# Optimization experiments

Hardware: AMD Instinct MI355X
Metric: run time of the kernel (lower is better)

The kernel has to match this reference:

```python
import jax, jax.numpy as jnp
import numpy as np

K_NEIGHBORS = 5
WEIGHT = 0.5
EPS = 1e-12


def _l2_normalize(x):
    return x / jnp.maximum(jnp.linalg.norm(x, axis=1, keepdims=True), EPS)


def setup_inputs() -> dict:
    key = jax.random.key(0)
    k1, k2, k3, k4 = jax.random.split(key, 4)
    return {
        "hidden_current": jax.random.normal(k1, (4096, 768), dtype=jnp.float32),
        "hidden_previous": jax.random.normal(k2, (8192, 768), dtype=jnp.float32),
        "labels_current": jax.random.randint(k3, (4096,), 0, 100, dtype=jnp.int64),
        "labels_previous": jax.random.randint(k4, (8192,), 0, 100, dtype=jnp.int64),
    }


def reference(hidden_current, hidden_previous, labels_current, labels_previous):
    B_curr = hidden_current.shape[0]
    B_prev = hidden_previous.shape[0]

    # --- affinity from previous representations (no_grad in original) ---
    hp = _l2_normalize(jax.lax.stop_gradient(hidden_previous))
    dist_prev = 1.0 - hp @ hp.T                      # [B_prev, B_prev] cosine distance
    # smallest k+1 distances == largest k+1 of negated distances
    _, nbr = jax.lax.top_k(-dist_prev, K_NEIGHBORS + 1)
    nbr = nbr[:, 1:]                                 # drop self, [B_prev, K]
    same = labels_previous[:, None] == labels_previous[nbr]   # [B_prev, K]
    e = jnp.where(same, 1.0, -1.0).astype(jnp.float32)        # w - b
    rows = jnp.arange(B_prev)[:, None]
    affinity = jnp.zeros((B_prev, B_prev), dtype=jnp.float32).at[rows, nbr].set(e)

    # --- squared pairwise distances of normalized current representations ---
    hc = _l2_normalize(hidden_current)
    sq = jnp.sum(hc * hc, axis=1)
    d2 = jnp.maximum(sq[:, None] + sq[None, :] - 2.0 * (hc @ hc.T), 0.0)  # [B_curr, B_curr]

    loss = jnp.sum(affinity[:B_curr, :B_curr] * d2) / (B_curr * B_curr)
    return WEIGHT * loss
```

## Files before the change

kernel.cpp:

```cpp
#include <hip/hip_runtime.h>

#define BC 4096
#define BP 8192
#define D  768
#define KNB 5
#define TOPK 6
#define NT (BP / 128)

typedef __bf16 bf16x8 __attribute__((ext_vector_type(8)));
typedef float  f32x4  __attribute__((ext_vector_type(4)));

__device__ __forceinline__ unsigned short f2bf(float f) {
    unsigned int u = __float_as_uint(f);
    u += 0x7fffu + ((u >> 16) & 1u);
    return (unsigned short)(u >> 16);
}

__device__ __forceinline__ void gload16(const void* g, void* l) {
    __builtin_amdgcn_global_load_lds(
        (const __attribute__((address_space(1))) unsigned int*)g,
        (__attribute__((address_space(3))) unsigned int*)l, 16, 0, 0);
}

__device__ __forceinline__ void topk_insert(float v, int j, float* bv, int* bj) {
    #pragma unroll
    for (int q = TOPK - 1; q >= 1; q--) {
        bool up   = v > bv[q - 1];
        bool here = (v > bv[q]) && !up;
        bv[q] = up ? bv[q - 1] : (here ? v : bv[q]);
        bj[q] = up ? bj[q - 1] : (here ? j : bj[q]);
    }
    if (v > bv[0]) { bv[0] = v; bj[0] = j; }
}

__global__ __launch_bounds__(256) void k_norm(const float* __restrict__ hp,
                                              const float* __restrict__ hc,
                                              unsigned short* __restrict__ hpnb,
                                              float* __restrict__ hcn,
                                              float* __restrict__ sqout,
                                              float* __restrict__ out) {
    int b = blockIdx.x;
    int t = threadIdx.x;
    if (b == 0 && t == 0) out[0] = 0.0f;
    bool isP = (b < BP);
    int row = isP ? b : (b - BP);
    const float* xr = (isP ? hp : hc) + (size_t)row * D;
    float v0 = xr[t], v1 = xr[t + 256], v2 = xr[t + 512];
    float s = v0 * v0 + v1 * v1 + v2 * v2;
    #pragma unroll
    for (int off = 32; off; off >>= 1) s += __shfl_xor(s, off, 64);
    __shared__ float wsum[4];
    if ((t & 63) == 0) wsum[t >> 6] = s;
    __syncthreads();
    float tot = wsum[0] + wsum[1] + wsum[2] + wsum[3];
    float rinv = 1.0f / fmaxf(sqrtf(tot), 1e-12f);
    if (isP) {
        unsigned short* yr = hpnb + (size_t)row * D;
        int rx = (row & 7) << 3;
        yr[t ^ rx]         = f2bf(v0 * rinv);
        yr[(t + 256) ^ rx] = f2bf(v1 * rinv);
        yr[(t + 512) ^ rx] = f2bf(v2 * rinv);
    } else {
        float* yr = hcn + (size_t)row * D;
        yr[t] = v0 * rinv; yr[t + 256] = v1 * rinv; yr[t + 512] = v2 * rinv;
        if (t == 0) sqout[row] = tot * rinv * rinv;
    }
}

__global__ __launch_bounds__(256, 3) void k_simtop(const unsigned short* __restrict__ hp,
                                                   float* __restrict__ candv,
                                                   int* __restrict__ candi) {
    __shared__ char smem[39424];
    unsigned short* sA = (unsigned short*)smem;
    unsigned short* sB = sA + 128 * 64;
    float* sS = (float*)smem;
    float* mv = (float*)(smem + 33280);
    int*   mj = (int*)(smem + 33280 + 3072);

    const int t = threadIdx.x;
    const int l = t & 63;
    const int w = t >> 6;
    const int l15 = l & 15, quad = l >> 4;
    const int wr = w >> 1, wc = w & 1;

    int ri, ci;
    {
        int b = blockIdx.x;
        int super_id = (((b >> 9) & 3) << 3) | (b & 7);
        int within = (b >> 3) & 63;
        ri = (super_id >> 3) * 8 + (within >> 3);
        ci = (super_id & 7) * 8 + (within & 7);
    }

    const int srow = l >> 3, sch = l & 7;
    const unsigned short* Ag = hp + (size_t)(ri * 128 + w * 32 + srow) * D + sch * 8;
    const unsigned short* Bg = hp + (size_t)(ci * 128 + w * 32 + srow) * D + sch * 8;
    unsigned short* la = sA + (w * 32) * 64;
    unsigned short* lb = sB + (w * 32) * 64;

    f32x4 acc[4][4];
    #pragma unroll
    for (int i = 0; i < 4; i++)
        #pragma unroll
        for (int j = 0; j < 4; j++) acc[i][j] = (f32x4){0.f, 0.f, 0.f, 0.f};

    const int x7  = l15 & 7;
    const int ch0 = (quad ^ x7) * 16;
    const int ch1 = ((quad + 4) ^ x7) * 16;

    for (int kk = 0; kk < D; kk += 64) {
        __syncthreads();
        #pragma unroll
        for (int p = 0; p < 4; p++) {
            gload16(Ag + (size_t)(p * 8) * D + kk, la + (p * 8) * 64);
            gload16(Bg + (size_t)(p * 8) * D + kk, lb + (p * 8) * 64);
        }
        __syncthreads();
        #pragma unroll
        for (int ks = 0; ks < 2; ks++) {
            const int ch = ks ? ch1 : ch0;
            bf16x8 af[4], bfr[4];
            #pragma unroll
            for (int mi = 0; mi < 4; mi++)
                af[mi] = *(const bf16x8*)((const char*)sA + (wr * 64 + mi * 16 + l15) * 128 + ch);
            #pragma unroll
            for (int ni = 0; ni < 4; ni++)
                bfr[ni] = *(const bf16x8*)((const char*)sB + (wc * 64 + ni * 16 + l15) * 128 + ch);
            #pragma unroll
            for (int mi = 0; mi < 4; mi++)
                #pragma unroll
                for (int ni = 0; ni < 4; ni++)
                    acc[mi][ni] = __builtin_amdgcn_mfma_f32_16x16x32_bf16(af[mi], bfr[ni], acc[mi][ni], 0, 0, 0);
        }
    }

    float bv[TOPK]; int bj[TOPK];
    #pragma unroll
    for (int s = 0; s < TOPK; s++) { bv[s] = -1e30f; bj[s] = 0x7fffffff; }

    const int erow = t & 127, scb = (t >> 7) * 32;
    #pragma unroll
    for (int h = 0; h < 2; h++) {
        __syncthreads();
        if (wc == h) {
            #pragma unroll
            for (int mi = 0; mi < 4; mi++)
                #pragma unroll
                for (int ni = 0; ni < 4; ni++) {
                    int colb = ni * 16 + l15;
                    int rowb = wr * 64 + mi * 16 + quad * 4;
                    f32x4 v = acc[mi][ni];
                    #pragma unroll
                    for (int r = 0; r < 4; r++) sS[(rowb + r) * 65 + colb] = v[r];
                }
        }
        __syncthreads();
        int jbase = ci * 128 + h * 64 + scb;
        for (int c = 0; c < 32; c++) {
            float v = sS[erow * 65 + scb + c];
            if (v > bv[TOPK - 1]) topk_insert(v, jbase + c, bv, bj);
        }
    }

    __syncthreads();
    if (t >= 128) {
        #pragma unroll
        for (int s = 0; s < TOPK; s++) { mv[(t - 128) * TOPK + s] = bv[s]; mj[(t - 128) * TOPK + s] = bj[s]; }
    }
    __syncthreads();
    if (t < 128) {
        #pragma unroll
        for (int s0 = 0; s0 < TOPK; s0++) {
            float v = mv[t * TOPK + s0];
            if (v > bv[TOPK - 1]) topk_insert(v, mj[t * TOPK + s0], bv, bj);
        }
        size_t o = ((size_t)(ri * 128 + t) * NT + ci) * TOPK;
        #pragma unroll
        for (int s = 0; s < TOPK; s++) { candv[o + s] = bv[s]; candi[o + s] = bj[s]; }
    }
}

__global__ __launch_bounds__(256) void k_mergeloss(const float* __restrict__ candv,
                                                   const int* __restrict__ candi,
                                                   const float* __restrict__ hcn,
                                                   const float* __restrict__ sq,
                                                   const int* __restrict__ labp,
                                                   float* __restrict__ out) {
    __shared__ float bsum[4];
    const int w = threadIdx.x >> 6, lane = threadIdx.x & 63;
    const int i = blockIdx.x * 4 + w;

    const float* cv = candv + ((size_t)i * NT + lane) * TOPK;
    const int*   cj = candi + ((size_t)i * NT + lane) * TOPK;
    float bv[TOPK]; int bj[TOPK];
    #pragma unroll
    for (int s = 0; s < TOPK; s++) { bv[s] = cv[s]; bj[s] = cj[s]; }

    #pragma unroll
    for (int off = 1; off < 64; off <<= 1) {
        float pv[TOPK]; int pj[TOPK];
        #pragma unroll
        for (int s = 0; s < TOPK; s++) {
            pv[s] = __shfl_xor(bv[s], off, 64);
            pj[s] = __shfl_xor(bj[s], off, 64);
        }
        bool ilow = (lane & off) == 0;
        float av[TOPK], iv[TOPK]; int aj[TOPK], ij[TOPK];
        #pragma unroll
        for (int s = 0; s < TOPK; s++) {
            av[s] = ilow ? bv[s] : pv[s];  aj[s] = ilow ? bj[s] : pj[s];
            iv[s] = ilow ? pv[s] : bv[s];  ij[s] = ilow ? pj[s] : bj[s];
        }
        #pragma unroll
        for (int s = 0; s < TOPK; s++)
            if (iv[s] > av[TOPK - 1]) topk_insert(iv[s], ij[s], av, aj);
        #pragma unroll
        for (int s = 0; s < TOPK; s++) { bv[s] = av[s]; bj[s] = aj[s]; }
    }

    const float* hi = hcn + (size_t)i * D;
    float4 h0 = *(const float4*)(hi + lane * 4);
    float4 h1 = *(const float4*)(hi + lane * 4 + 256);
    float4 h2 = *(const float4*)(hi + lane * 4 + 512);
    float sqi = sq[i];
    int li = labp[i];
    float part = 0.f;
    float base = 0.f;
    #pragma unroll
    for (int s = 1; s <= KNB; s++) {
        int j = bj[s];
        if (j >= BC) continue;
        const float* hj = hcn + (size_t)j * D;
        float4 g0 = *(const float4*)(hj + lane * 4);
        float4 g1 = *(const float4*)(hj + lane * 4 + 256);
        float4 g2 = *(const float4*)(hj + lane * 4 + 512);
        float d = h0.x * g0.x + h0.y * g0.y + h0.z * g0.z + h0.w * g0.w
                + h1.x * g1.x + h1.y * g1.y + h1.z * g1.z + h1.w * g1.w
                + h2.x * g2.x + h2.y * g2.y + h2.z * g2.z + h2.w * g2.w;
        float e = (li == labp[j]) ? 1.0f : -1.0f;
        part += e * (-2.0f) * d;
        if (lane == 0) base += e * (sqi + sq[j]);
    }
    part += base;
    #pragma unroll
    for (int off = 32; off; off >>= 1) part += __shfl_xor(part, off, 64);
    if (lane == 0) bsum[w] = part;
    __syncthreads();
    if (threadIdx.x == 0) {
        float s = bsum[0] + bsum[1] + bsum[2] + bsum[3];
        unsafeAtomicAdd(out, 0.5f * s / ((float)BC * (float)BC));
    }
}

extern "C" void kernel_launch(void* const* d_in, const int* in_sizes, int n_in,
                              void* d_out, int out_size, void* d_ws, size_t ws_size,
                              hipStream_t stream) {
    const float* hc   = (const float*)d_in[0];
    const float* hp   = (const float*)d_in[1];
    const int*   labp = (const int*)d_in[3];
    float* out = (float*)d_out;

    unsigned short* hpnb = (unsigned short*)d_ws;
    float* hcn  = (float*)(hpnb + (size_t)BP * D);
    float* sq   = hcn + (size_t)BC * D;
    float* candv = sq + BC;
    int*   candi = (int*)(candv + (size_t)BC * NT * TOPK);

    k_norm<<<dim3(BP + BC), dim3(256), 0, stream>>>(hp, hc, hpnb, hcn, sq, out);
    k_simtop<<<dim3(2048), dim3(256), 0, stream>>>(hpnb, candv, candi);
    k_mergeloss<<<dim3(BC / 4), dim3(256), 0, stream>>>(candv, candi, hcn, sq, labp, out);
}
```

Measured before the change: 183.1 us.

## Pack similarity value and column index into one unsigned top-k key

Offsets the dot-product accumulators by 4 so every similarity is positive. Each value is then packed with a reversed 7-bit column index into a single unsigned key, which makes the top-k insertion a branchless compare on one register instead of parallel float/index arrays. This also shrinks shared memory, allowing occupancy to be raised to 4 blocks per SIMD, and it wraps the MFMA loop in s_setprio. The cost is that the low 7 mantissa bits of each similarity are truncated, which can change neighbour order for near-ties, and the top-k scan is now fully unrolled with no early-exit branch.

```diff
diff --git a/kernel.cpp b/kernel.cpp
--- a/kernel.cpp
+++ b/kernel.cpp
@@ -31,6 +31,16 @@
         bj[q] = up ? bj[q - 1] : (here ? j : bj[q]);
     }
     if (v > bv[0]) { bv[0] = v; bj[0] = j; }
+}
+
+__device__ __forceinline__ void topk_insert_u(unsigned v, unsigned* bk) {
+    #pragma unroll
+    for (int q = TOPK - 1; q >= 1; q--) {
+        bool up   = v > bk[q - 1];
+        bool here = (v > bk[q]) && !up;
+        bk[q] = up ? bk[q - 1] : (here ? v : bk[q]);
+    }
+    if (v > bk[0]) bk[0] = v;
 }
 
 __global__ __launch_bounds__(256) void k_norm(const float* __restrict__ hp,
@@ -67,15 +77,14 @@
     }
 }
 
-__global__ __launch_bounds__(256, 3) void k_simtop(const unsigned short* __restrict__ hp,
+__global__ __launch_bounds__(256, 4) void k_simtop(const unsigned short* __restrict__ hp,
                                                    float* __restrict__ candv,
                                                    int* __restrict__ candi) {
-    __shared__ char smem[39424];
+    __shared__ char smem[36864];
     unsigned short* sA = (unsigned short*)smem;
     unsigned short* sB = sA + 128 * 64;
-    float* sS = (float*)smem;
-    float* mv = (float*)(smem + 33280);
-    int*   mj = (int*)(smem + 33280 + 3072);
+    unsigned* sK = (unsigned*)smem;
+    unsigned* mk = (unsigned*)(smem + 33280);
 
     const int t = threadIdx.x;
     const int l = t & 63;
@@ -102,7 +111,7 @@
     #pragma unroll
     for (int i = 0; i < 4; i++)
         #pragma unroll
-        for (int j = 0; j < 4; j++) acc[i][j] = (f32x4){0.f, 0.f, 0.f, 0.f};
+        for (int j = 0; j < 4; j++) acc[i][j] = (f32x4){4.f, 4.f, 4.f, 4.f};
 
     const int x7  = l15 & 7;
     const int ch0 = (quad ^ x7) * 16;
@@ -126,17 +135,19 @@
             #pragma unroll
             for (int ni = 0; ni < 4; ni++)
                 bfr[ni] = *(const bf16x8*)((const char*)sB + (wc * 64 + ni * 16 + l15) * 128 + ch);
+            __builtin_amdgcn_s_setprio(1);
             #pragma unroll
             for (int mi = 0; mi < 4; mi++)
                 #pragma unroll
                 for (int ni = 0; ni < 4; ni++)
                     acc[mi][ni] = __builtin_amdgcn_mfma_f32_16x16x32_bf16(af[mi], bfr[ni], acc[mi][ni], 0, 0, 0);
-        }
-    }
-
-    float bv[TOPK]; int bj[TOPK];
-    #pragma unroll
-    for (int s = 0; s < TOPK; s++) { bv[s] = -1e30f; bj[s] = 0x7fffffff; }
+            __builtin_amdgcn_s_setprio(0);
+        }
+    }
+
+    unsigned bk[TOPK];
+    #pragma unroll
+    for (int s = 0; s < TOPK; s++) bk[s] = 0u;
 
     const int erow = t & 127, scb = (t >> 7) * 32;
     #pragma unroll
@@ -144,39 +155,42 @@
         __syncthreads();
         if (wc == h) {
             #pragma unroll
-            for (int mi = 0; mi < 4; mi++)
+            for (int ni = 0; ni < 4; ni++) {
+                unsigned pk = (unsigned)(127 - h * 64 - ni * 16 - l15);
                 #pragma unroll
-                for (int ni = 0; ni < 4; ni++) {
+                for (int mi = 0; mi < 4; mi++) {
                     int colb = ni * 16 + l15;
                     int rowb = wr * 64 + mi * 16 + quad * 4;
                     f32x4 v = acc[mi][ni];
                     #pragma unroll
-                    for (int r = 0; r < 4; r++) sS[(rowb + r) * 65 + colb] = v[r];
+                    for (int r = 0; r < 4; r++)
+                        sK[(rowb + r) * 65 + colb] =
+                            (__float_as_uint(v[r]) & 0xFFFFFF80u) | pk;
                 }
-        }
-        __syncthreads();
-        int jbase = ci * 128 + h * 64 + scb;
-        for (int c = 0; c < 32; c++) {
-            float v = sS[erow * 65 + scb + c];
-            if (v > bv[TOPK - 1]) topk_insert(v, jbase + c, bv, bj);
-        }
+            }
+        }
+        __syncthreads();
+        const unsigned* rowp = sK + erow * 65 + scb;
+        #pragma unroll
+        for (int c = 0; c < 32; c++) topk_insert_u(rowp[c], bk);
     }
 
     __syncthreads();
     if (t >= 128) {
         #pragma unroll
-        for (int s = 0; s < TOPK; s++) { mv[(t - 128) * TOPK + s] = bv[s]; mj[(t - 128) * TOPK + s] = bj[s]; }
+        for (int s = 0; s < TOPK; s++) mk[(t - 128) * 7 + s] = bk[s];
     }
     __syncthreads();
     if (t < 128) {
         #pragma unroll
-        for (int s0 = 0; s0 < TOPK; s0++) {
-            float v = mv[t * TOPK + s0];
-            if (v > bv[TOPK - 1]) topk_insert(v, mj[t * TOPK + s0], bv, bj);
-        }
+        for (int s0 = 0; s0 < TOPK; s0++) topk_insert_u(mk[t * 7 + s0], bk);
         size_t o = ((size_t)(ri * 128 + t) * NT + ci) * TOPK;
         #pragma unroll
-        for (int s = 0; s < TOPK; s++) { candv[o + s] = bv[s]; candi[o + s] = bj[s]; }
+        for (int s = 0; s < TOPK; s++) {
+            unsigned k = bk[s];
+            candv[o + s] = __uint_as_float(k & 0xFFFFFF80u);
+            candi[o + s] = ci * 128 + 127 - (int)(k & 127u);
+        }
     }
 }
 
```

New measurement: 160.7 us. -12.2%, faster.
